# Kernel optimization log

Hardware: AMD Instinct MI355X
Metric: run time of the kernel (lower is better)

Reference implementation:

```python
import jax, jax.numpy as jnp
import numpy as np

WS = 7
HEADS = 8
DIM = 256
IN_DIM = 128
HID = 1024
EPS = 1e-5


def _rel_index(ws):
    coords = np.stack(np.meshgrid(np.arange(ws), np.arange(ws), indexing='ij'))  # (2,ws,ws)
    cf = coords.reshape(2, -1)                      # (2,N)
    rel = (cf[:, :, None] - cf[:, None, :]).transpose(1, 2, 0).copy()  # (N,N,2)
    rel[..., 0] += ws - 1
    rel[..., 1] += ws - 1
    rel[..., 0] *= 2 * ws - 1
    return rel.sum(-1)  # (N,N) int

REL_IDX = jnp.asarray(_rel_index(WS).reshape(-1))


def layernorm(x, g, b):
    mu = jnp.mean(x, axis=-1, keepdims=True)
    var = jnp.mean(jnp.square(x - mu), axis=-1, keepdims=True)
    return (x - mu) * jax.lax.rsqrt(var + EPS) * g + b


def setup_inputs() -> dict:
    key = jax.random.key(0)
    ks = jax.random.split(key, 16)
    s = 0.02
    return {
        'x': jax.random.normal(ks[0], (16, IN_DIM, 56, 56), jnp.float32),
        'conv_w': jax.random.normal(ks[1], (DIM, IN_DIM, 3, 3), jnp.float32) * s,
        'conv_b': jnp.zeros((DIM,), jnp.float32),
        'g1': jnp.ones((DIM,), jnp.float32), 'b1': jnp.zeros((DIM,), jnp.float32),
        'g2': jnp.ones((DIM,), jnp.float32), 'b2': jnp.zeros((DIM,), jnp.float32),
        'g3': jnp.ones((DIM,), jnp.float32), 'b3': jnp.zeros((DIM,), jnp.float32),
        'qkv_w': jax.random.normal(ks[2], (3 * DIM, DIM), jnp.float32) * s,
        'rel_bias_table': jax.random.normal(ks[3], ((2 * WS - 1) ** 2, HEADS), jnp.float32) * s,
        'proj_w': jax.random.normal(ks[4], (DIM, DIM), jnp.float32) * s,
        'proj_b': jnp.zeros((DIM,), jnp.float32),
        'fc1_w': jax.random.normal(ks[5], (HID, DIM), jnp.float32) * s,
        'fc1_b': jnp.zeros((HID,), jnp.float32),
        'fc2_w': jax.random.normal(ks[6], (DIM, HID), jnp.float32) * s,
        'fc2_b': jnp.zeros((DIM,), jnp.float32),
    }


def reference(x, conv_w, conv_b, g1, b1, g2, b2, g3, b3, qkv_w, rel_bias_table,
              proj_w, proj_b, fc1_w, fc1_b, fc2_w, fc2_b):
    # proj_q: 3x3 conv, stride 1, pad 1 (input_dim != embed_dim)
    x = jax.lax.conv_general_dilated(
        x, conv_w, window_strides=(1, 1), padding=((1, 1), (1, 1)),
        dimension_numbers=('NCHW', 'OIHW', 'NCHW')) + conv_b[None, :, None, None]
    b, c, h, w = x.shape
    x = x.reshape(b, c, h * w).transpose(0, 2, 1)  # (b, n, c)
    x = layernorm(x, g1, b1)
    x = x.reshape(b, h, w, c)
    pb = (WS - h % WS) % WS
    pr = (WS - w % WS) % WS
    x = jnp.pad(x, ((0, 0), (0, pb), (0, pr), (0, 0)))
    hp, wp = h + pb, w + pr
    # window partition -> (nW, N, c)
    xw = x.reshape(b, hp // WS, WS, wp // WS, WS, c)
    xw = xw.transpose(0, 1, 3, 2, 4, 5).reshape(-1, WS * WS, c)
    nW, N, _ = xw.shape
    d = c // HEADS
    qkv = (xw @ qkv_w.T).reshape(nW, N, 3, HEADS, d).transpose(2, 0, 3, 1, 4)  # (3,nW,h,N,d)
    q, k, v = qkv[0] * (d ** -0.5), qkv[1], qkv[2]
    attn = jnp.einsum('whnd,whmd->whnm', q, k)
    bias = rel_bias_table[REL_IDX].reshape(N, N, HEADS).transpose(2, 0, 1)  # (h,N,N)
    attn = jax.nn.softmax(attn + bias[None], axis=-1)
    out = jnp.einsum('whnm,whmd->whnd', attn, v).transpose(0, 2, 1, 3).reshape(nW, N, c)
    out = out @ proj_w.T + proj_b
    # window reverse
    x = out.reshape(b, hp // WS, wp // WS, WS, WS, c)
    x = x.transpose(0, 1, 3, 2, 4, 5).reshape(b, hp, wp, c)
    x = x[:, :h, :w, :].reshape(b, h * w, c)
    # NOTE: faithful to source — NO residual from pre-attention stream
    x = layernorm(x, g2, b2)
    x = jax.nn.gelu(x @ fc1_w.T + fc1_b, approximate=False) @ fc2_w.T + fc2_b
    x = x + x  # source: x = x + drop_path(x) with identity drop_path
    x = layernorm(x, g3, b3)
    return x.reshape(b, h, w, c).transpose(0, 3, 1, 2)
```

## Files before the change

### kernel.cpp

```cpp
#include <hip/hip_runtime.h>
#include <hip/hip_bf16.h>

typedef unsigned short u16;
typedef unsigned int   u32;

#define TTOK  50176
#define CDIM  256

using short8 = __attribute__((ext_vector_type(8))) short;
using f32x4  = __attribute__((ext_vector_type(4))) float;

__device__ __forceinline__ float b2f(u16 u) { return __uint_as_float(((u32)u) << 16); }
__device__ __forceinline__ u16 f2b(float f) {
    u32 x = __float_as_uint(f);
    return (u16)((x + 0x7fffu + ((x >> 16) & 1u)) >> 16);
}

#define GLD16(src, dst) __builtin_amdgcn_global_load_lds( \
    (const __attribute__((address_space(1))) void*)(src),  \
    (__attribute__((address_space(3))) void*)(dst), 16, 0, 0)

__global__ __launch_bounds__(256) void cvt_k(const float* __restrict__ in, u16* __restrict__ out, int n4) {
    int i = blockIdx.x * 256 + threadIdx.x;
    if (i >= n4) return;
    float4 v = *(const float4*)&in[i * 4];
    ushort4 o;
    o.x = f2b(v.x); o.y = f2b(v.y); o.z = f2b(v.z); o.w = f2b(v.w);
    *(ushort4*)&out[i * 4] = o;
}

__global__ __launch_bounds__(256) void pad_k(const float* __restrict__ x, u16* __restrict__ xp) {
    __shared__ float tile[128][58];
    int bid = blockIdx.x;
    int b = bid / 58, hp = bid - b * 58;
    int tid = threadIdx.x;
    bool zrow = (hp == 0 || hp == 57);
    if (!zrow) {
        int h = hp - 1;
        for (int e = tid; e < 128 * 14; e += 256) {
            int ic = e / 14, j = e - ic * 14;
            float4 v = *(const float4*)&x[(((size_t)b * 128 + ic) * 56 + h) * 56 + j * 4];
            tile[ic][j * 4 + 0] = v.x; tile[ic][j * 4 + 1] = v.y;
            tile[ic][j * 4 + 2] = v.z; tile[ic][j * 4 + 3] = v.w;
        }
        __syncthreads();
    }
    size_t rb = ((size_t)b * 58 + hp) * 58 * 128;
    for (int u = tid; u < 58 * 16; u += 256) {
        int wp = u / 16, icg = u - wp * 16;
        uint4 o = make_uint4(0u, 0u, 0u, 0u);
        if (!zrow && wp != 0 && wp != 57) {
            int w = wp - 1, ic0 = icg * 8;
            u16 v0 = f2b(tile[ic0 + 0][w]), v1 = f2b(tile[ic0 + 1][w]);
            u16 v2 = f2b(tile[ic0 + 2][w]), v3 = f2b(tile[ic0 + 3][w]);
            u16 v4 = f2b(tile[ic0 + 4][w]), v5 = f2b(tile[ic0 + 5][w]);
            u16 v6 = f2b(tile[ic0 + 6][w]), v7 = f2b(tile[ic0 + 7][w]);
            o.x = (u32)v0 | ((u32)v1 << 16);
            o.y = (u32)v2 | ((u32)v3 << 16);
            o.z = (u32)v4 | ((u32)v5 << 16);
            o.w = (u32)v6 | ((u32)v7 << 16);
        }
        *(uint4*)&xp[rb + (size_t)wp * 128 + icg * 8] = o;
    }
}

__global__ __launch_bounds__(256) void w2_k(const float* __restrict__ w, u16* __restrict__ o2) {
    int e = blockIdx.x * 256 + threadIdx.x;
    int o = e / 1152, rem = e - o * 1152;
    int tap = rem >> 7, ic = rem & 127;
    o2[e] = f2b(w[(o * 128 + ic) * 9 + tap]);
}

__device__ __forceinline__ void xcd_remap(int& bx, int& by) {
    int nx = gridDim.x, ny = gridDim.y;
    if ((ny & 7) == 0) {
        int linear = blockIdx.y * nx + blockIdx.x;
        int xcd = linear & 7, within = linear >> 3;
        bx = within % nx;
        by = xcd * (ny >> 3) + within / nx;
    } else { bx = blockIdx.x; by = blockIdx.y; }
}

__global__ __launch_bounds__(256) void gemm_conv_k(const u16* __restrict__ xp, const u16* __restrict__ W2,
                                                   const float* __restrict__ bias, u16* __restrict__ C) {
    __shared__ __align__(16) u16 lsA[128 * 64];
    __shared__ __align__(16) u16 lsB[128 * 64];
    int tid = threadIdx.x;
    int wave = tid >> 6, lane = tid & 63;
    int bx, by; xcd_remap(bx, by);
    int mBase = by * 128, nBase = bx * 128;
    int wm = wave >> 1, wn = wave & 1;
    int lr = lane & 15, lq = lane >> 4;
    int r8 = lane >> 3, kg = lane & 7;
    int kgsw = ((kg ^ r8) & 7) * 8;

    size_t tb[4]; const u16* gB[4];
#pragma unroll
    for (int i = 0; i < 4; ++i) {
        int t = mBase + (wave * 4 + i) * 8 + r8;
        int win = t / 49, n = t - win * 49;
        int b = win >> 6, wh = (win >> 3) & 7, ww = win & 7;
        int r = n / 7, s = n - r * 7;
        tb[i] = ((size_t)(b * 58 + wh * 7 + r) * 58 + ww * 7 + s) * 128 + kgsw;
        gB[i] = W2 + (size_t)(nBase + (wave * 4 + i) * 8 + r8) * 1152 + kgsw;
    }

    f32x4 acc[4][4];
#pragma unroll
    for (int m = 0; m < 4; ++m)
#pragma unroll
        for (int n = 0; n < 4; ++n) acc[m][n] = (f32x4){0.f, 0.f, 0.f, 0.f};

    for (int ks = 0; ks < 18; ++ks) {
        int tap = ks >> 1, half = ks & 1;
        int kh = tap / 3, kw = tap - kh * 3;
        int uoff = (kh * 58 + kw) * 128 + half * 64;
#pragma unroll
        for (int i = 0; i < 4; ++i) {
            int crow = wave * 4 + i;
            GLD16(xp + tb[i] + uoff, lsA + crow * 512);
            GLD16(gB[i] + ks * 64,   lsB + crow * 512);
        }
        __syncthreads();
#pragma unroll
        for (int kk = 0; kk < 2; ++kk) {
            int sl = (((kk << 2) | lq) ^ (lr & 7)) * 8;
            short8 af[4], bf[4];
#pragma unroll
            for (int m = 0; m < 4; ++m)
                af[m] = *(const short8*)&lsA[(wm * 64 + m * 16 + lr) * 64 + sl];
#pragma unroll
            for (int n = 0; n < 4; ++n)
                bf[n] = *(const short8*)&lsB[(wn * 64 + n * 16 + lr) * 64 + sl];
#pragma unroll
            for (int m = 0; m < 4; ++m)
#pragma unroll
                for (int n = 0; n < 4; ++n)
                    acc[m][n] = __builtin_amdgcn_mfma_f32_16x16x32_bf16(af[m], bf[n], acc[m][n], 0, 0, 0);
        }
        __syncthreads();
    }

#pragma unroll
    for (int m = 0; m < 4; ++m) {
        int row0 = mBase + wm * 64 + m * 16 + lq * 4;
#pragma unroll
        for (int n = 0; n < 4; ++n) {
            int col = nBase + wn * 64 + n * 16 + lr;
            float bv = bias[col];
#pragma unroll
            for (int r = 0; r < 4; ++r)
                C[(size_t)(row0 + r) * 256 + col] = f2b(acc[m][n][r] + bv);
        }
    }
}

template <int EPI>
__global__ __launch_bounds__(256) void gemm_k(const u16* __restrict__ A, const u16* __restrict__ Bw,
                                              const float* __restrict__ bias, u16* __restrict__ C,
                                              int M, int N, int K) {
    __shared__ __align__(16) u16 lsA[128 * 64];
    __shared__ __align__(16) u16 lsB[128 * 64];
    int tid = threadIdx.x;
    int wave = tid >> 6, lane = tid & 63;
    int bx, by; xcd_remap(bx, by);
    int mBase = by * 128, nBase = bx * 128;
    int wm = wave >> 1, wn = wave & 1;
    int lr = lane & 15, lq = lane >> 4;
    int r8 = lane >> 3, kg = lane & 7;
    int kgsw = ((kg ^ r8) & 7) * 8;

    const u16* gA[4]; const u16* gB[4];
#pragma unroll
    for (int i = 0; i < 4; ++i) {
        int crow = wave * 4 + i;
        gA[i] = A  + (size_t)(mBase + crow * 8 + r8) * K + kgsw;
        gB[i] = Bw + (size_t)(nBase + crow * 8 + r8) * K + kgsw;
    }

    f32x4 acc[4][4];
#pragma unroll
    for (int m = 0; m < 4; ++m)
#pragma unroll
        for (int n = 0; n < 4; ++n) acc[m][n] = (f32x4){0.f, 0.f, 0.f, 0.f};

    for (int k0 = 0; k0 < K; k0 += 64) {
#pragma unroll
        for (int i = 0; i < 4; ++i) {
            int crow = wave * 4 + i;
            GLD16(gA[i] + k0, lsA + crow * 512);
            GLD16(gB[i] + k0, lsB + crow * 512);
        }
        __syncthreads();
#pragma unroll
        for (int kk = 0; kk < 2; ++kk) {
            int sl = (((kk << 2) | lq) ^ (lr & 7)) * 8;
            short8 af[4], bf[4];
#pragma unroll
            for (int m = 0; m < 4; ++m)
                af[m] = *(const short8*)&lsA[(wm * 64 + m * 16 + lr) * 64 + sl];
#pragma unroll
            for (int n = 0; n < 4; ++n)
                bf[n] = *(const short8*)&lsB[(wn * 64 + n * 16 + lr) * 64 + sl];
#pragma unroll
            for (int m = 0; m < 4; ++m)
#pragma unroll
                for (int n = 0; n < 4; ++n)
                    acc[m][n] = __builtin_amdgcn_mfma_f32_16x16x32_bf16(af[m], bf[n], acc[m][n], 0, 0, 0);
        }
        __syncthreads();
    }

#pragma unroll
    for (int m = 0; m < 4; ++m) {
        int row0 = mBase + wm * 64 + m * 16 + lq * 4;
#pragma unroll
        for (int n = 0; n < 4; ++n) {
            int col = nBase + wn * 64 + n * 16 + lr;
            float bv = (EPI >= 1) ? bias[col] : 0.f;
#pragma unroll
            for (int r = 0; r < 4; ++r) {
                float v = acc[m][n][r] + bv;
                if (EPI == 2) v = 0.5f * v * (1.f + erff(v * 0.70710678118654752f));
                C[(size_t)(row0 + r) * N + col] = f2b(v);
            }
        }
    }
}

__global__ __launch_bounds__(256) void ln_k(u16* __restrict__ y, const float* __restrict__ g,
                                            const float* __restrict__ bta) {
    int wid = (blockIdx.x << 2) + (threadIdx.x >> 6);
    int lane = threadIdx.x & 63;
    u16* row = y + (size_t)wid * CDIM;
    ushort4 u = *(const ushort4*)&row[lane * 4];
    float v0 = b2f(u.x), v1 = b2f(u.y), v2 = b2f(u.z), v3 = b2f(u.w);
    float s = v0 + v1 + v2 + v3;
    float q = v0 * v0 + v1 * v1 + v2 * v2 + v3 * v3;
#pragma unroll
    for (int o = 32; o; o >>= 1) { s += __shfl_xor(s, o); q += __shfl_xor(q, o); }
    float mean = s * (1.f / 256.f);
    float var = q * (1.f / 256.f) - mean * mean;
    float inv = rsqrtf(var + 1e-5f);
    float4 gg = *(const float4*)&g[lane * 4];
    float4 bb = *(const float4*)&bta[lane * 4];
    ushort4 o4;
    o4.x = f2b((v0 - mean) * inv * gg.x + bb.x);
    o4.y = f2b((v1 - mean) * inv * gg.y + bb.y);
    o4.z = f2b((v2 - mean) * inv * gg.z + bb.z);
    o4.w = f2b((v3 - mean) * inv * gg.w + bb.w);
    *(ushort4*)&row[lane * 4] = o4;
}

__global__ __launch_bounds__(256) void attn_mfma_k(const u16* __restrict__ qkv,
                                                   const float* __restrict__ tab,
                                                   u16* __restrict__ out) {
    __shared__ __align__(16) u16 sh[28488];
    int tid = threadIdx.x;
    int wave = tid >> 6, lane = tid & 63;
    int wh = blockIdx.x * 4 + wave;
    int win = wh >> 3, head = wh & 7;
    int g = lane >> 4, cc = lane & 15;

    u16* Pl = sh + wave * 4608;
    u16* Vl = sh + 18432 + wave * 2176;
    float* bs = (float*)(sh + 27136) + wave * 169;

    const size_t wbase = (size_t)win * 49 * 768;
    for (int e = lane; e < 169; e += 64) bs[e] = tab[e * 8 + head];
    for (int e = lane; e < 49 * 16; e += 64) {
        int k = e >> 4, d0 = (e & 15) * 2;
        *(u32*)&Vl[k * 34 + d0] = *(const u32*)&qkv[wbase + (size_t)k * 768 + 512 + head * 32 + d0];
    }
    for (int e = lane; e < 15 * 16; e += 64) {
        int k = 49 + (e >> 4), d0 = (e & 15) * 2;
        *(u32*)&Vl[k * 34 + d0] = 0u;
    }
    __syncthreads();

    short8 aQ[4], bK[4];
#pragma unroll
    for (int t = 0; t < 4; ++t) {
        int qr = t * 16 + cc; if (qr > 48) qr = 48;
        aQ[t] = *(const short8*)&qkv[wbase + (size_t)qr * 768 + head * 32 + g * 8];
        int kr = t * 16 + cc; if (kr > 48) kr = 48;
        bK[t] = *(const short8*)&qkv[wbase + (size_t)kr * 768 + 256 + head * 32 + g * 8];
    }
    f32x4 S[4][4];
#pragma unroll
    for (int a = 0; a < 4; ++a)
#pragma unroll
        for (int b = 0; b < 4; ++b)
            S[a][b] = __builtin_amdgcn_mfma_f32_16x16x32_bf16(aQ[a], bK[b], (f32x4){0.f,0.f,0.f,0.f}, 0, 0, 0);

    int AqA[4][4];
#pragma unroll
    for (int tr = 0; tr < 4; ++tr)
#pragma unroll
        for (int r = 0; r < 4; ++r) {
            int q = tr * 16 + g * 4 + r; if (q > 48) q = 48;
            int dq = (q * 37) >> 8;
            AqA[tr][r] = 6 * dq + q + 84;
        }
    int AcA[4];
    bool colBad[4];
#pragma unroll
    for (int tc = 0; tc < 4; ++tc) {
        int c = tc * 16 + cc;
        colBad[tc] = (c > 48);
        if (c > 48) c = 48;
        int dc = (c * 37) >> 8;
        AcA[tc] = 6 * dc + c;
    }
    const float scale = 0.17677669529663687f;
    float inv[4][4];
#pragma unroll
    for (int tr = 0; tr < 4; ++tr) {
#pragma unroll
        for (int r = 0; r < 4; ++r) {
            float z0 = colBad[0] ? -1e30f : S[tr][0][r] * scale + bs[AqA[tr][r] - AcA[0]];
            float z1 = colBad[1] ? -1e30f : S[tr][1][r] * scale + bs[AqA[tr][r] - AcA[1]];
            float z2 = colBad[2] ? -1e30f : S[tr][2][r] * scale + bs[AqA[tr][r] - AcA[2]];
            float z3 = colBad[3] ? -1e30f : S[tr][3][r] * scale + bs[AqA[tr][r] - AcA[3]];
            float mx = fmaxf(fmaxf(z0, z1), fmaxf(z2, z3));
            mx = fmaxf(mx, __shfl_xor(mx, 1));
            mx = fmaxf(mx, __shfl_xor(mx, 2));
            mx = fmaxf(mx, __shfl_xor(mx, 4));
            mx = fmaxf(mx, __shfl_xor(mx, 8));
            float p0 = __expf(z0 - mx), p1 = __expf(z1 - mx);
            float p2 = __expf(z2 - mx), p3 = __expf(z3 - mx);
            S[tr][0][r] = p0; S[tr][1][r] = p1; S[tr][2][r] = p2; S[tr][3][r] = p3;
            float sm = p0 + p1 + p2 + p3;
            sm += __shfl_xor(sm, 1); sm += __shfl_xor(sm, 2);
            sm += __shfl_xor(sm, 4); sm += __shfl_xor(sm, 8);
            inv[tr][r] = 1.0f / sm;
        }
    }

#pragma unroll
    for (int tr = 0; tr < 4; ++tr)
#pragma unroll
        for (int tc = 0; tc < 4; ++tc) {
            int k = tc * 16 + cc;
            u16* pb = &Pl[tr * 1152 + k * 18 + g * 4];
            u32 w0 = (u32)f2b(S[tr][tc][0]) | ((u32)f2b(S[tr][tc][1]) << 16);
            u32 w1 = (u32)f2b(S[tr][tc][2]) | ((u32)f2b(S[tr][tc][3]) << 16);
            *(u32*)pb = w0;
            *(u32*)(pb + 2) = w1;
        }
    __syncthreads();

    f32x4 O[4][2];
#pragma unroll
    for (int a = 0; a < 4; ++a) { O[a][0] = (f32x4){0.f,0.f,0.f,0.f}; O[a][1] = (f32x4){0.f,0.f,0.f,0.f}; }
#pragma unroll
    for (int s = 0; s < 2; ++s) {
        short8 pa[4], vb[2];
#pragma unroll
        for (int tr = 0; tr < 4; ++tr)
#pragma unroll
            for (int j = 0; j < 8; ++j)
                pa[tr][j] = (short)Pl[tr * 1152 + (s * 32 + g * 8 + j) * 18 + cc];
#pragma unroll
        for (int td = 0; td < 2; ++td)
#pragma unroll
            for (int j = 0; j < 8; ++j)
                vb[td][j] = (short)Vl[(s * 32 + g * 8 + j) * 34 + td * 16 + cc];
#pragma unroll
        for (int tr = 0; tr < 4; ++tr)
#pragma unroll
            for (int td = 0; td < 2; ++td)
                O[tr][td] = __builtin_amdgcn_mfma_f32_16x16x32_bf16(pa[tr], vb[td], O[tr][td], 0, 0, 0);
    }

#pragma unroll
    for (int tr = 0; tr < 4; ++tr)
#pragma unroll
        for (int r = 0; r < 4; ++r) {
            int q = tr * 16 + g * 4 + r;
            if (q < 49) {
                float iv = inv[tr][r];
                u16* op = out + (size_t)(win * 49 + q) * 256 + head * 32;
                op[cc]      = f2b(O[tr][0][r] * iv);
                op[16 + cc] = f2b(O[tr][1][r] * iv);
            }
        }
}

__global__ __launch_bounds__(256) void ln3_out_k(const u16* __restrict__ f, const float* __restrict__ g3,
                                                 const float* __restrict__ b3, float* __restrict__ out) {
    __shared__ float tile[256][57];
    int bh = blockIdx.x;
    int b = bh / 56, h = bh - b * 56;
    int wv = threadIdx.x >> 6, lane = threadIdx.x & 63;
    int wh = h / 7, r = h - wh * 7;
    float4 gg = *(const float4*)&g3[lane * 4];
    float4 bb = *(const float4*)&b3[lane * 4];
    for (int i = 0; i < 14; ++i) {
        int w = wv + i * 4;
        int wwn = w / 7, s2 = w - wwn * 7;
        int t = (b * 64 + wh * 8 + wwn) * 49 + r * 7 + s2;
        ushort4 u = *(const ushort4*)&f[(size_t)t * 256 + lane * 4];
        float v0 = 2.f * b2f(u.x), v1 = 2.f * b2f(u.y), v2 = 2.f * b2f(u.z), v3 = 2.f * b2f(u.w);
        float s = v0 + v1 + v2 + v3;
        float q = v0 * v0 + v1 * v1 + v2 * v2 + v3 * v3;
#pragma unroll
        for (int o = 32; o; o >>= 1) { s += __shfl_xor(s, o); q += __shfl_xor(q, o); }
        float mean = s * (1.f / 256.f);
        float var = q * (1.f / 256.f) - mean * mean;
        float inv = rsqrtf(var + 1e-5f);
        int c = lane * 4;
        tile[c + 0][w] = (v0 - mean) * inv * gg.x + bb.x;
        tile[c + 1][w] = (v1 - mean) * inv * gg.y + bb.y;
        tile[c + 2][w] = (v2 - mean) * inv * gg.z + bb.z;
        tile[c + 3][w] = (v3 - mean) * inv * gg.w + bb.w;
    }
    __syncthreads();
    size_t obase = (size_t)b * 256 * 3136 + (size_t)h * 56;
#pragma unroll
    for (int it = 0; it < 28; ++it) {
        int e = it * 256 + threadIdx.x;
        int c = e / 28, wu = e - c * 28;
        float2 pack = make_float2(tile[c][wu * 2], tile[c][wu * 2 + 1]);
        *(float2*)&out[obase + (size_t)c * 3136 + wu * 2] = pack;
    }
}

extern "C" void kernel_launch(void* const* d_in, const int* in_sizes, int n_in,
                              void* d_out, int out_size, void* d_ws, size_t ws_size,
                              hipStream_t stream) {
    (void)in_sizes; (void)n_in; (void)out_size;
    const float* x      = (const float*)d_in[0];
    const float* conv_w = (const float*)d_in[1];
    const float* conv_b = (const float*)d_in[2];
    const float* g1     = (const float*)d_in[3];
    const float* b1     = (const float*)d_in[4];
    const float* g2     = (const float*)d_in[5];
    const float* b2     = (const float*)d_in[6];
    const float* g3     = (const float*)d_in[7];
    const float* b3     = (const float*)d_in[8];
    const float* qkv_w  = (const float*)d_in[9];
    const float* tab    = (const float*)d_in[10];
    const float* proj_w = (const float*)d_in[11];
    const float* proj_b = (const float*)d_in[12];
    const float* fc1_w  = (const float*)d_in[13];
    const float* fc1_b  = (const float*)d_in[14];
    const float* fc2_w  = (const float*)d_in[15];
    const float* fc2_b  = (const float*)d_in[16];
    float* outp = (float*)d_out;

    const size_t OFF_Y  = (size_t)TTOK * 1152 * 2;
    const size_t OFF_AT = OFF_Y + (size_t)TTOK * 512;
    const size_t NEED   = OFF_AT + (size_t)TTOK * 512;
    if (ws_size < NEED) return;

    char* ws = (char*)d_ws;
    u16* xpad    = (u16*)ws;
    u16* ybuf    = (u16*)(ws + OFF_Y);
    u16* atout   = (u16*)(ws + OFF_AT);
    u16* qkvbuf  = (u16*)ws;
    u16* hidden  = (u16*)ws;
    u16* W2      = atout;
    u16* wbase   = (u16*)(ws + (size_t)TTOK * 1024 * 2);
    u16* qkvw_b  = wbase;
    u16* projw_b = wbase + 196608;
    u16* fc1w_b  = projw_b + 65536;
    u16* fc2w_b  = fc1w_b + 262144;

    pad_k<<<928, 256, 0, stream>>>(x, xpad);
    w2_k<<<1152, 256, 0, stream>>>(conv_w, W2);
    cvt_k<<<192, 256, 0, stream>>>(qkv_w, qkvw_b, 49152);
    cvt_k<<<64,  256, 0, stream>>>(proj_w, projw_b, 16384);
    cvt_k<<<256, 256, 0, stream>>>(fc1_w, fc1w_b, 65536);
    cvt_k<<<256, 256, 0, stream>>>(fc2_w, fc2w_b, 65536);
    gemm_conv_k<<<dim3(2, 392), 256, 0, stream>>>(xpad, W2, conv_b, ybuf);
    ln_k<<<12544, 256, 0, stream>>>(ybuf, g1, b1);
    gemm_k<0><<<dim3(6, 392), 256, 0, stream>>>(ybuf, qkvw_b, nullptr, qkvbuf, TTOK, 768, 256);
    attn_mfma_k<<<2048, 256, 0, stream>>>(qkvbuf, tab, atout);
    gemm_k<1><<<dim3(2, 392), 256, 0, stream>>>(atout, projw_b, proj_b, ybuf, TTOK, 256, 256);
    ln_k<<<12544, 256, 0, stream>>>(ybuf, g2, b2);
    gemm_k<2><<<dim3(8, 392), 256, 0, stream>>>(ybuf, fc1w_b, fc1_b, hidden, TTOK, 1024, 256);
    gemm_k<1><<<dim3(2, 392), 256, 0, stream>>>(hidden, fc2w_b, fc2_b, atout, TTOK, 256, 1024);
    ln3_out_k<<<896, 256, 0, stream>>>(atout, g3, b3, outp);
}
```

Measured before the change: 332.6 us.

## Enlarge GEMM tiles to 256x256 with 8 waves and generalize XCD remap

All GEMM kernels (conv and linear) move from 128x128 tiles with 4 waves to 256x256 tiles with 8 waves of 512 threads. Each wave now computes a 128x64 sub-tile, which raises MFMA work per LDS fragment load and halves global traffic per output. The XCD remap now handles grid sizes that are not a multiple of 8. In exchange the grid shrinks to 196 M-blocks, fewer than 256 CUs, so occupancy and wave balance may suffer, and 64KB of LDS plus 128 accumulator registers per thread raise resource pressure.

```diff
diff --git a/kernel.cpp b/kernel.cpp
--- a/kernel.cpp
+++ b/kernel.cpp
@@ -73,41 +73,41 @@
 
 __device__ __forceinline__ void xcd_remap(int& bx, int& by) {
     int nx = gridDim.x, ny = gridDim.y;
-    if ((ny & 7) == 0) {
-        int linear = blockIdx.y * nx + blockIdx.x;
-        int xcd = linear & 7, within = linear >> 3;
-        bx = within % nx;
-        by = xcd * (ny >> 3) + within / nx;
-    } else { bx = blockIdx.x; by = blockIdx.y; }
-}
-
-__global__ __launch_bounds__(256) void gemm_conv_k(const u16* __restrict__ xp, const u16* __restrict__ W2,
+    int total = nx * ny;
+    int lin = blockIdx.y * nx + blockIdx.x;
+    int q = total >> 3, r = total & 7;
+    int xcd = lin & 7, idx = lin >> 3;
+    int wgid = (xcd < r ? xcd * (q + 1) : r * (q + 1) + (xcd - r) * q) + idx;
+    by = wgid / nx; bx = wgid - by * nx;
+}
+
+__global__ __launch_bounds__(512) void gemm_conv_k(const u16* __restrict__ xp, const u16* __restrict__ W2,
                                                    const float* __restrict__ bias, u16* __restrict__ C) {
-    __shared__ __align__(16) u16 lsA[128 * 64];
-    __shared__ __align__(16) u16 lsB[128 * 64];
+    __shared__ __align__(16) u16 lsA[256 * 64];
+    __shared__ __align__(16) u16 lsB[256 * 64];
     int tid = threadIdx.x;
     int wave = tid >> 6, lane = tid & 63;
     int bx, by; xcd_remap(bx, by);
-    int mBase = by * 128, nBase = bx * 128;
-    int wm = wave >> 1, wn = wave & 1;
+    int mBase = by * 256, nBase = bx * 256;
+    int wm = wave >> 2, wn = wave & 3;
     int lr = lane & 15, lq = lane >> 4;
-    int r8 = lane >> 3, kg = lane & 7;
-    int kgsw = ((kg ^ r8) & 7) * 8;
+    int r8 = tid >> 3, kg = tid & 7;
+    int kgsw = ((kg ^ (r8 & 7)) & 7) * 8;
 
     size_t tb[4]; const u16* gB[4];
 #pragma unroll
     for (int i = 0; i < 4; ++i) {
-        int t = mBase + (wave * 4 + i) * 8 + r8;
+        int t = mBase + i * 64 + r8;
         int win = t / 49, n = t - win * 49;
         int b = win >> 6, wh = (win >> 3) & 7, ww = win & 7;
         int r = n / 7, s = n - r * 7;
         tb[i] = ((size_t)(b * 58 + wh * 7 + r) * 58 + ww * 7 + s) * 128 + kgsw;
-        gB[i] = W2 + (size_t)(nBase + (wave * 4 + i) * 8 + r8) * 1152 + kgsw;
-    }
-
-    f32x4 acc[4][4];
-#pragma unroll
-    for (int m = 0; m < 4; ++m)
+        gB[i] = W2 + (size_t)(nBase + i * 64 + r8) * 1152 + kgsw;
+    }
+
+    f32x4 acc[8][4];
+#pragma unroll
+    for (int m = 0; m < 8; ++m)
 #pragma unroll
         for (int n = 0; n < 4; ++n) acc[m][n] = (f32x4){0.f, 0.f, 0.f, 0.f};
 
@@ -117,23 +117,22 @@
         int uoff = (kh * 58 + kw) * 128 + half * 64;
 #pragma unroll
         for (int i = 0; i < 4; ++i) {
-            int crow = wave * 4 + i;
-            GLD16(xp + tb[i] + uoff, lsA + crow * 512);
-            GLD16(gB[i] + ks * 64,   lsB + crow * 512);
+            GLD16(xp + tb[i] + uoff, lsA + (i * 64 + wave * 8) * 64);
+            GLD16(gB[i] + ks * 64,   lsB + (i * 64 + wave * 8) * 64);
         }
         __syncthreads();
 #pragma unroll
         for (int kk = 0; kk < 2; ++kk) {
             int sl = (((kk << 2) | lq) ^ (lr & 7)) * 8;
-            short8 af[4], bf[4];
-#pragma unroll
-            for (int m = 0; m < 4; ++m)
-                af[m] = *(const short8*)&lsA[(wm * 64 + m * 16 + lr) * 64 + sl];
+            short8 af[8], bf[4];
+#pragma unroll
+            for (int m = 0; m < 8; ++m)
+                af[m] = *(const short8*)&lsA[(wm * 128 + m * 16 + lr) * 64 + sl];
 #pragma unroll
             for (int n = 0; n < 4; ++n)
                 bf[n] = *(const short8*)&lsB[(wn * 64 + n * 16 + lr) * 64 + sl];
 #pragma unroll
-            for (int m = 0; m < 4; ++m)
+            for (int m = 0; m < 8; ++m)
 #pragma unroll
                 for (int n = 0; n < 4; ++n)
                     acc[m][n] = __builtin_amdgcn_mfma_f32_16x16x32_bf16(af[m], bf[n], acc[m][n], 0, 0, 0);
@@ -142,8 +141,8 @@
     }
 
 #pragma unroll
-    for (int m = 0; m < 4; ++m) {
-        int row0 = mBase + wm * 64 + m * 16 + lq * 4;
+    for (int m = 0; m < 8; ++m) {
+        int row0 = mBase + wm * 128 + m * 16 + lq * 4;
 #pragma unroll
         for (int n = 0; n < 4; ++n) {
             int col = nBase + wn * 64 + n * 16 + lr;
@@ -156,54 +155,52 @@
 }
 
 template <int EPI>
-__global__ __launch_bounds__(256) void gemm_k(const u16* __restrict__ A, const u16* __restrict__ Bw,
+__global__ __launch_bounds__(512) void gemm_k(const u16* __restrict__ A, const u16* __restrict__ Bw,
                                               const float* __restrict__ bias, u16* __restrict__ C,
                                               int M, int N, int K) {
-    __shared__ __align__(16) u16 lsA[128 * 64];
-    __shared__ __align__(16) u16 lsB[128 * 64];
+    __shared__ __align__(16) u16 lsA[256 * 64];
+    __shared__ __align__(16) u16 lsB[256 * 64];
     int tid = threadIdx.x;
     int wave = tid >> 6, lane = tid & 63;
     int bx, by; xcd_remap(bx, by);
-    int mBase = by * 128, nBase = bx * 128;
-    int wm = wave >> 1, wn = wave & 1;
+    int mBase = by * 256, nBase = bx * 256;
+    int wm = wave >> 2, wn = wave & 3;
     int lr = lane & 15, lq = lane >> 4;
-    int r8 = lane >> 3, kg = lane & 7;
-    int kgsw = ((kg ^ r8) & 7) * 8;
+    int r8 = tid >> 3, kg = tid & 7;
+    int kgsw = ((kg ^ (r8 & 7)) & 7) * 8;
 
     const u16* gA[4]; const u16* gB[4];
 #pragma unroll
     for (int i = 0; i < 4; ++i) {
-        int crow = wave * 4 + i;
-        gA[i] = A  + (size_t)(mBase + crow * 8 + r8) * K + kgsw;
-        gB[i] = Bw + (size_t)(nBase + crow * 8 + r8) * K + kgsw;
-    }
-
-    f32x4 acc[4][4];
-#pragma unroll
-    for (int m = 0; m < 4; ++m)
+        gA[i] = A  + (size_t)(mBase + i * 64 + r8) * K + kgsw;
+        gB[i] = Bw + (size_t)(nBase + i * 64 + r8) * K + kgsw;
+    }
+
+    f32x4 acc[8][4];
+#pragma unroll
+    for (int m = 0; m < 8; ++m)
 #pragma unroll
         for (int n = 0; n < 4; ++n) acc[m][n] = (f32x4){0.f, 0.f, 0.f, 0.f};
 
     for (int k0 = 0; k0 < K; k0 += 64) {
 #pragma unroll
         for (int i = 0; i < 4; ++i) {
-            int crow = wave * 4 + i;
-            GLD16(gA[i] + k0, lsA + crow * 512);
-            GLD16(gB[i] + k0, lsB + crow * 512);
+            GLD16(gA[i] + k0, lsA + (i * 64 + wave * 8) * 64);
+            GLD16(gB[i] + k0, lsB + (i * 64 + wave * 8) * 64);
         }
         __syncthreads();
 #pragma unroll
         for (int kk = 0; kk < 2; ++kk) {
             int sl = (((kk << 2) | lq) ^ (lr & 7)) * 8;
-            short8 af[4], bf[4];
-#pragma unroll
-            for (int m = 0; m < 4; ++m)
-                af[m] = *(const short8*)&lsA[(wm * 64 + m * 16 + lr) * 64 + sl];
+            short8 af[8], bf[4];
+#pragma unroll
+            for (int m = 0; m < 8; ++m)
+                af[m] = *(const short8*)&lsA[(wm * 128 + m * 16 + lr) * 64 + sl];
 #pragma unroll
             for (int n = 0; n < 4; ++n)
                 bf[n] = *(const short8*)&lsB[(wn * 64 + n * 16 + lr) * 64 + sl];
 #pragma unroll
-            for (int m = 0; m < 4; ++m)
+            for (int m = 0; m < 8; ++m)
 #pragma unroll
                 for (int n = 0; n < 4; ++n)
                     acc[m][n] = __builtin_amdgcn_mfma_f32_16x16x32_bf16(af[m], bf[n], acc[m][n], 0, 0, 0);
@@ -212,8 +209,8 @@
     }
 
 #pragma unroll
-    for (int m = 0; m < 4; ++m) {
-        int row0 = mBase + wm * 64 + m * 16 + lq * 4;
+    for (int m = 0; m < 8; ++m) {
+        int row0 = mBase + wm * 128 + m * 16 + lq * 4;
 #pragma unroll
         for (int n = 0; n < 4; ++n) {
             int col = nBase + wn * 64 + n * 16 + lr;
@@ -473,13 +470,13 @@
     cvt_k<<<64,  256, 0, stream>>>(proj_w, projw_b, 16384);
     cvt_k<<<256, 256, 0, stream>>>(fc1_w, fc1w_b, 65536);
     cvt_k<<<256, 256, 0, stream>>>(fc2_w, fc2w_b, 65536);
-    gemm_conv_k<<<dim3(2, 392), 256, 0, stream>>>(xpad, W2, conv_b, ybuf);
+    gemm_conv_k<<<dim3(1, 196), 512, 0, stream>>>(xpad, W2, conv_b, ybuf);
     ln_k<<<12544, 256, 0, stream>>>(ybuf, g1, b1);
-    gemm_k<0><<<dim3(6, 392), 256, 0, stream>>>(ybuf, qkvw_b, nullptr, qkvbuf, TTOK, 768, 256);
+    gemm_k<0><<<dim3(3, 196), 512, 0, stream>>>(ybuf, qkvw_b, nullptr, qkvbuf, TTOK, 768, 256);
     attn_mfma_k<<<2048, 256, 0, stream>>>(qkvbuf, tab, atout);
-    gemm_k<1><<<dim3(2, 392), 256, 0, stream>>>(atout, projw_b, proj_b, ybuf, TTOK, 256, 256);
+    gemm_k<1><<<dim3(1, 196), 512, 0, stream>>>(atout, projw_b, proj_b, ybuf, TTOK, 256, 256);
     ln_k<<<12544, 256, 0, stream>>>(ybuf, g2, b2);
-    gemm_k<2><<<dim3(8, 392), 256, 0, stream>>>(ybuf, fc1w_b, fc1_b, hidden, TTOK, 1024, 256);
-    gemm_k<1><<<dim3(2, 392), 256, 0, stream>>>(hidden, fc2w_b, fc2_b, atout, TTOK, 256, 1024);
+    gemm_k<2><<<dim3(4, 196), 512, 0, stream>>>(ybuf, fc1w_b, fc1_b, hidden, TTOK, 1024, 256);
+    gemm_k<1><<<dim3(1, 196), 512, 0, stream>>>(hidden, fc2w_b, fc2_b, atout, TTOK, 256, 1024);
     ln3_out_k<<<896, 256, 0, stream>>>(atout, g3, b3, outp);
 }
```

After: 360.1 us. +8.3%, slower.

## Fuse LayerNorm into conv and proj GEMM epilogues with full-row N tiles

Applied to the files above, without the earlier changes.

Widens the conv GEMM and the attention-projection GEMM so each block covers all 256 output columns, then computes the LayerNorm statistics in the epilogue through shuffles and a small LDS reduction. This drops two standalone LayerNorm passes that each read and wrote the full activation buffer. It also merges the four weight-conversion launches into one kernel. In exchange the fused kernels hold twice the accumulators (128 floats per thread) and launch only 392 blocks, which may lower occupancy and leave the device underfilled.

```diff
diff --git a/kernel.cpp b/kernel.cpp
--- a/kernel.cpp
+++ b/kernel.cpp
@@ -20,13 +20,19 @@
     (const __attribute__((address_space(1))) void*)(src),  \
     (__attribute__((address_space(3))) void*)(dst), 16, 0, 0)
 
-__global__ __launch_bounds__(256) void cvt_k(const float* __restrict__ in, u16* __restrict__ out, int n4) {
+__global__ __launch_bounds__(256) void cvt4_k(const float* __restrict__ a, const float* __restrict__ b,
+                                              const float* __restrict__ c, const float* __restrict__ d,
+                                              u16* __restrict__ dst) {
     int i = blockIdx.x * 256 + threadIdx.x;
-    if (i >= n4) return;
-    float4 v = *(const float4*)&in[i * 4];
+    const float* src; int off;
+    if (i < 49152)       { src = a; off = i; }
+    else if (i < 65536)  { src = b; off = i - 49152; }
+    else if (i < 131072) { src = c; off = i - 65536; }
+    else                 { src = d; off = i - 131072; }
+    float4 v = *(const float4*)&src[off * 4];
     ushort4 o;
     o.x = f2b(v.x); o.y = f2b(v.y); o.z = f2b(v.z); o.w = f2b(v.w);
-    *(ushort4*)&out[i * 4] = o;
+    *(ushort4*)&dst[i * 4] = o;
 }
 
 __global__ __launch_bounds__(256) void pad_k(const float* __restrict__ x, u16* __restrict__ xp) {
@@ -81,78 +87,225 @@
     } else { bx = blockIdx.x; by = blockIdx.y; }
 }
 
-__global__ __launch_bounds__(256) void gemm_conv_k(const u16* __restrict__ xp, const u16* __restrict__ W2,
-                                                   const float* __restrict__ bias, u16* __restrict__ C) {
+__device__ __forceinline__ int xcd_remap1d() {
+    int nb = gridDim.x, lin = blockIdx.x;
+    int q = nb >> 3, r = nb & 7;
+    int xcd = lin & 7, idx = lin >> 3;
+    return (xcd < r ? xcd * (q + 1) : r * (q + 1) + (xcd - r) * q) + idx;
+}
+
+__global__ __launch_bounds__(256) void gemm_conv_ln_k(const u16* __restrict__ xp, const u16* __restrict__ W2,
+                                                      const float* __restrict__ bias,
+                                                      const float* __restrict__ gam, const float* __restrict__ bet,
+                                                      u16* __restrict__ C) {
     __shared__ __align__(16) u16 lsA[128 * 64];
-    __shared__ __align__(16) u16 lsB[128 * 64];
+    __shared__ __align__(16) u16 lsB[256 * 64];
     int tid = threadIdx.x;
     int wave = tid >> 6, lane = tid & 63;
-    int bx, by; xcd_remap(bx, by);
-    int mBase = by * 128, nBase = bx * 128;
+    int by = xcd_remap1d();
+    int mBase = by * 128;
     int wm = wave >> 1, wn = wave & 1;
     int lr = lane & 15, lq = lane >> 4;
-    int r8 = lane >> 3, kg = lane & 7;
-    int kgsw = ((kg ^ r8) & 7) * 8;
-
-    size_t tb[4]; const u16* gB[4];
-#pragma unroll
-    for (int i = 0; i < 4; ++i) {
-        int t = mBase + (wave * 4 + i) * 8 + r8;
+    int rr = lane >> 3, kg = lane & 7;
+    int kgsw = ((kg ^ rr) & 7) * 8;
+
+    size_t tb[4]; const u16* gB[8];
+#pragma unroll
+    for (int j = 0; j < 4; ++j) {
+        int t = mBase + wave * 32 + j * 8 + rr;
         int win = t / 49, n = t - win * 49;
         int b = win >> 6, wh = (win >> 3) & 7, ww = win & 7;
         int r = n / 7, s = n - r * 7;
-        tb[i] = ((size_t)(b * 58 + wh * 7 + r) * 58 + ww * 7 + s) * 128 + kgsw;
-        gB[i] = W2 + (size_t)(nBase + (wave * 4 + i) * 8 + r8) * 1152 + kgsw;
-    }
-
-    f32x4 acc[4][4];
-#pragma unroll
-    for (int m = 0; m < 4; ++m)
-#pragma unroll
-        for (int n = 0; n < 4; ++n) acc[m][n] = (f32x4){0.f, 0.f, 0.f, 0.f};
+        tb[j] = ((size_t)(b * 58 + wh * 7 + r) * 58 + ww * 7 + s) * 128 + kgsw;
+    }
+#pragma unroll
+    for (int j = 0; j < 8; ++j)
+        gB[j] = W2 + (size_t)(wave * 64 + j * 8 + rr) * 1152 + kgsw;
+
+    f32x4 acc[4][8];
+#pragma unroll
+    for (int m = 0; m < 4; ++m)
+#pragma unroll
+        for (int n = 0; n < 8; ++n) acc[m][n] = (f32x4){0.f, 0.f, 0.f, 0.f};
 
     for (int ks = 0; ks < 18; ++ks) {
         int tap = ks >> 1, half = ks & 1;
         int kh = tap / 3, kw = tap - kh * 3;
         int uoff = (kh * 58 + kw) * 128 + half * 64;
 #pragma unroll
-        for (int i = 0; i < 4; ++i) {
-            int crow = wave * 4 + i;
-            GLD16(xp + tb[i] + uoff, lsA + crow * 512);
-            GLD16(gB[i] + ks * 64,   lsB + crow * 512);
-        }
+        for (int j = 0; j < 4; ++j) GLD16(xp + tb[j] + uoff, lsA + (wave * 32 + j * 8) * 64);
+#pragma unroll
+        for (int j = 0; j < 8; ++j) GLD16(gB[j] + ks * 64, lsB + (wave * 64 + j * 8) * 64);
         __syncthreads();
 #pragma unroll
         for (int kk = 0; kk < 2; ++kk) {
             int sl = (((kk << 2) | lq) ^ (lr & 7)) * 8;
-            short8 af[4], bf[4];
+            short8 af[4], bf[8];
 #pragma unroll
             for (int m = 0; m < 4; ++m)
                 af[m] = *(const short8*)&lsA[(wm * 64 + m * 16 + lr) * 64 + sl];
 #pragma unroll
-            for (int n = 0; n < 4; ++n)
-                bf[n] = *(const short8*)&lsB[(wn * 64 + n * 16 + lr) * 64 + sl];
+            for (int n = 0; n < 8; ++n)
+                bf[n] = *(const short8*)&lsB[(wn * 128 + n * 16 + lr) * 64 + sl];
 #pragma unroll
             for (int m = 0; m < 4; ++m)
 #pragma unroll
-                for (int n = 0; n < 4; ++n)
+                for (int n = 0; n < 8; ++n)
                     acc[m][n] = __builtin_amdgcn_mfma_f32_16x16x32_bf16(af[m], bf[n], acc[m][n], 0, 0, 0);
         }
         __syncthreads();
     }
 
-#pragma unroll
-    for (int m = 0; m < 4; ++m) {
-        int row0 = mBase + wm * 64 + m * 16 + lq * 4;
-#pragma unroll
-        for (int n = 0; n < 4; ++n) {
-            int col = nBase + wn * 64 + n * 16 + lr;
-            float bv = bias[col];
-#pragma unroll
-            for (int r = 0; r < 4; ++r)
-                C[(size_t)(row0 + r) * 256 + col] = f2b(acc[m][n][r] + bv);
-        }
-    }
+    float bv[8], gv[8], btv[8];
+#pragma unroll
+    for (int n = 0; n < 8; ++n) {
+        int col = wn * 128 + n * 16 + lr;
+        bv[n] = bias[col]; gv[n] = gam[col]; btv[n] = bet[col];
+    }
+#pragma unroll
+    for (int m = 0; m < 4; ++m)
+#pragma unroll
+        for (int n = 0; n < 8; ++n)
+#pragma unroll
+            for (int r = 0; r < 4; ++r) acc[m][n][r] += bv[n];
+
+    float* red = (float*)lsA;
+#pragma unroll
+    for (int m = 0; m < 4; ++m)
+#pragma unroll
+        for (int r = 0; r < 4; ++r) {
+            float s = 0.f, qq = 0.f;
+#pragma unroll
+            for (int n = 0; n < 8; ++n) { float v = acc[m][n][r]; s += v; qq += v * v; }
+            s += __shfl_xor(s, 1); s += __shfl_xor(s, 2); s += __shfl_xor(s, 4); s += __shfl_xor(s, 8);
+            qq += __shfl_xor(qq, 1); qq += __shfl_xor(qq, 2); qq += __shfl_xor(qq, 4); qq += __shfl_xor(qq, 8);
+            if (lr == 0) {
+                int row = wm * 64 + m * 16 + lq * 4 + r;
+                red[row * 4 + wn * 2] = s; red[row * 4 + wn * 2 + 1] = qq;
+            }
+        }
+    __syncthreads();
+
+#pragma unroll
+    for (int m = 0; m < 4; ++m)
+#pragma unroll
+        for (int r = 0; r < 4; ++r) {
+            int row = wm * 64 + m * 16 + lq * 4 + r;
+            float S = red[row * 4] + red[row * 4 + 2];
+            float Q = red[row * 4 + 1] + red[row * 4 + 3];
+            float mean = S * (1.f / 256.f);
+            float var = Q * (1.f / 256.f) - mean * mean;
+            float inv = rsqrtf(var + 1e-5f);
+            size_t grow = (size_t)(mBase + row) * 256;
+#pragma unroll
+            for (int n = 0; n < 8; ++n) {
+                int col = wn * 128 + n * 16 + lr;
+                C[grow + col] = f2b((acc[m][n][r] - mean) * inv * gv[n] + btv[n]);
+            }
+        }
+}
+
+__global__ __launch_bounds__(256) void gemm_ln_k(const u16* __restrict__ A, const u16* __restrict__ Bw,
+                                                 const float* __restrict__ bias,
+                                                 const float* __restrict__ gam, const float* __restrict__ bet,
+                                                 u16* __restrict__ C, int K) {
+    __shared__ __align__(16) u16 lsA[128 * 64];
+    __shared__ __align__(16) u16 lsB[256 * 64];
+    int tid = threadIdx.x;
+    int wave = tid >> 6, lane = tid & 63;
+    int by = xcd_remap1d();
+    int mBase = by * 128;
+    int wm = wave >> 1, wn = wave & 1;
+    int lr = lane & 15, lq = lane >> 4;
+    int rr = lane >> 3, kg = lane & 7;
+    int kgsw = ((kg ^ rr) & 7) * 8;
+
+    const u16* gA[4]; const u16* gB[8];
+#pragma unroll
+    for (int j = 0; j < 4; ++j)
+        gA[j] = A + (size_t)(mBase + wave * 32 + j * 8 + rr) * K + kgsw;
+#pragma unroll
+    for (int j = 0; j < 8; ++j)
+        gB[j] = Bw + (size_t)(wave * 64 + j * 8 + rr) * K + kgsw;
+
+    f32x4 acc[4][8];
+#pragma unroll
+    for (int m = 0; m < 4; ++m)
+#pragma unroll
+        for (int n = 0; n < 8; ++n) acc[m][n] = (f32x4){0.f, 0.f, 0.f, 0.f};
+
+    for (int k0 = 0; k0 < K; k0 += 64) {
+#pragma unroll
+        for (int j = 0; j < 4; ++j) GLD16(gA[j] + k0, lsA + (wave * 32 + j * 8) * 64);
+#pragma unroll
+        for (int j = 0; j < 8; ++j) GLD16(gB[j] + k0, lsB + (wave * 64 + j * 8) * 64);
+        __syncthreads();
+#pragma unroll
+        for (int kk = 0; kk < 2; ++kk) {
+            int sl = (((kk << 2) | lq) ^ (lr & 7)) * 8;
+            short8 af[4], bf[8];
+#pragma unroll
+            for (int m = 0; m < 4; ++m)
+                af[m] = *(const short8*)&lsA[(wm * 64 + m * 16 + lr) * 64 + sl];
+#pragma unroll
+            for (int n = 0; n < 8; ++n)
+                bf[n] = *(const short8*)&lsB[(wn * 128 + n * 16 + lr) * 64 + sl];
+#pragma unroll
+            for (int m = 0; m < 4; ++m)
+#pragma unroll
+                for (int n = 0; n < 8; ++n)
+                    acc[m][n] = __builtin_amdgcn_mfma_f32_16x16x32_bf16(af[m], bf[n], acc[m][n], 0, 0, 0);
+        }
+        __syncthreads();
+    }
+
+    float bv[8], gv[8], btv[8];
+#pragma unroll
+    for (int n = 0; n < 8; ++n) {
+        int col = wn * 128 + n * 16 + lr;
+        bv[n] = bias[col]; gv[n] = gam[col]; btv[n] = bet[col];
+    }
+#pragma unroll
+    for (int m = 0; m < 4; ++m)
+#pragma unroll
+        for (int n = 0; n < 8; ++n)
+#pragma unroll
+            for (int r = 0; r < 4; ++r) acc[m][n][r] += bv[n];
+
+    float* red = (float*)lsA;
+#pragma unroll
+    for (int m = 0; m < 4; ++m)
+#pragma unroll
+        for (int r = 0; r < 4; ++r) {
+            float s = 0.f, qq = 0.f;
+#pragma unroll
+            for (int n = 0; n < 8; ++n) { float v = acc[m][n][r]; s += v; qq += v * v; }
+            s += __shfl_xor(s, 1); s += __shfl_xor(s, 2); s += __shfl_xor(s, 4); s += __shfl_xor(s, 8);
+            qq += __shfl_xor(qq, 1); qq += __shfl_xor(qq, 2); qq += __shfl_xor(qq, 4); qq += __shfl_xor(qq, 8);
+            if (lr == 0) {
+                int row = wm * 64 + m * 16 + lq * 4 + r;
+                red[row * 4 + wn * 2] = s; red[row * 4 + wn * 2 + 1] = qq;
+            }
+        }
+    __syncthreads();
+
+#pragma unroll
+    for (int m = 0; m < 4; ++m)
+#pragma unroll
+        for (int r = 0; r < 4; ++r) {
+            int row = wm * 64 + m * 16 + lq * 4 + r;
+            float S = red[row * 4] + red[row * 4 + 2];
+            float Q = red[row * 4 + 1] + red[row * 4 + 3];
+            float mean = S * (1.f / 256.f);
+            float var = Q * (1.f / 256.f) - mean * mean;
+            float inv = rsqrtf(var + 1e-5f);
+            size_t grow = (size_t)(mBase + row) * 256;
+#pragma unroll
+            for (int n = 0; n < 8; ++n) {
+                int col = wn * 128 + n * 16 + lr;
+                C[grow + col] = f2b((acc[m][n][r] - mean) * inv * gv[n] + btv[n]);
+            }
+        }
 }
 
 template <int EPI>
@@ -226,30 +379,6 @@
             }
         }
     }
-}
-
-__global__ __launch_bounds__(256) void ln_k(u16* __restrict__ y, const float* __restrict__ g,
-                                            const float* __restrict__ bta) {
-    int wid = (blockIdx.x << 2) + (threadIdx.x >> 6);
-    int lane = threadIdx.x & 63;
-    u16* row = y + (size_t)wid * CDIM;
-    ushort4 u = *(const ushort4*)&row[lane * 4];
-    float v0 = b2f(u.x), v1 = b2f(u.y), v2 = b2f(u.z), v3 = b2f(u.w);
-    float s = v0 + v1 + v2 + v3;
-    float q = v0 * v0 + v1 * v1 + v2 * v2 + v3 * v3;
-#pragma unroll
-    for (int o = 32; o; o >>= 1) { s += __shfl_xor(s, o); q += __shfl_xor(q, o); }
-    float mean = s * (1.f / 256.f);
-    float var = q * (1.f / 256.f) - mean * mean;
-    float inv = rsqrtf(var + 1e-5f);
-    float4 gg = *(const float4*)&g[lane * 4];
-    float4 bb = *(const float4*)&bta[lane * 4];
-    ushort4 o4;
-    o4.x = f2b((v0 - mean) * inv * gg.x + bb.x);
-    o4.y = f2b((v1 - mean) * inv * gg.y + bb.y);
-    o4.z = f2b((v2 - mean) * inv * gg.z + bb.z);
-    o4.w = f2b((v3 - mean) * inv * gg.w + bb.w);
-    *(ushort4*)&row[lane * 4] = o4;
 }
 
 __global__ __launch_bounds__(256) void attn_mfma_k(const u16* __restrict__ qkv,
@@ -469,16 +598,11 @@
 
     pad_k<<<928, 256, 0, stream>>>(x, xpad);
     w2_k<<<1152, 256, 0, stream>>>(conv_w, W2);
-    cvt_k<<<192, 256, 0, stream>>>(qkv_w, qkvw_b, 49152);
-    cvt_k<<<64,  256, 0, stream>>>(proj_w, projw_b, 16384);
-    cvt_k<<<256, 256, 0, stream>>>(fc1_w, fc1w_b, 65536);
-    cvt_k<<<256, 256, 0, stream>>>(fc2_w, fc2w_b, 65536);
-    gemm_conv_k<<<dim3(2, 392), 256, 0, stream>>>(xpad, W2, conv_b, ybuf);
-    ln_k<<<12544, 256, 0, stream>>>(ybuf, g1, b1);
+    cvt4_k<<<768, 256, 0, stream>>>(qkv_w, proj_w, fc1_w, fc2_w, qkvw_b);
+    gemm_conv_ln_k<<<392, 256, 0, stream>>>(xpad, W2, conv_b, g1, b1, ybuf);
     gemm_k<0><<<dim3(6, 392), 256, 0, stream>>>(ybuf, qkvw_b, nullptr, qkvbuf, TTOK, 768, 256);
     attn_mfma_k<<<2048, 256, 0, stream>>>(qkvbuf, tab, atout);
-    gemm_k<1><<<dim3(2, 392), 256, 0, stream>>>(atout, projw_b, proj_b, ybuf, TTOK, 256, 256);
-    ln_k<<<12544, 256, 0, stream>>>(ybuf, g2, b2);
+    gemm_ln_k<<<392, 256, 0, stream>>>(atout, projw_b, proj_b, g2, b2, ybuf, 256);
     gemm_k<2><<<dim3(8, 392), 256, 0, stream>>>(ybuf, fc1w_b, fc1_b, hidden, TTOK, 1024, 256);
     gemm_k<1><<<dim3(2, 392), 256, 0, stream>>>(hidden, fc2w_b, fc2_b, atout, TTOK, 256, 1024);
     ln3_out_k<<<896, 256, 0, stream>>>(atout, g3, b3, outp);
```

After: 345.9 us. 1.04x slower.
